# Kernel tuning notes

Hardware: AMD Instinct MI355X
Metric: run time of the kernel (lower is better)

## Reference

```python
import jax, jax.numpy as jnp
import numpy as np

NEG_BIG = -1e12
ALPHA = 0.2  # LeakyReLU negative slope

def setup_inputs() -> dict:
    key = jax.random.key(0)
    k1, k2, k3, k4, k5 = jax.random.split(key, 5)
    N, F_in, F_out = 8192, 256, 128
    inp = jax.random.normal(k1, (N, F_in), dtype=jnp.float32)
    adj = jax.random.randint(k2, (N, N), 0, 2, dtype=jnp.int32)
    W = jax.random.normal(k3, (F_in, F_out), dtype=jnp.float32) * 0.05
    W_2 = jax.random.normal(k4, (F_in, F_out), dtype=jnp.float32) * 0.05
    W_3 = jax.random.normal(k5, (F_in, F_out), dtype=jnp.float32) * 0.05
    return {"inp": inp, "adj": adj, "W": W, "W_2": W_2, "W_3": W_3}

def reference(inp, adj, W, W_2, W_3):
    # h = inp @ W, h_2 = inp @ W_2  -> scores e = LeakyReLU(h @ h_2^T)  [N, N]
    h = inp @ W
    h_2 = inp @ W_2
    e = jax.nn.leaky_relu(h @ h_2.T, negative_slope=ALPHA)
    # adjacency mask, row softmax (dropout disabled: eval mode)
    attention = jax.nn.softmax(jnp.where(adj > 0, e, NEG_BIG), axis=1)
    h_3 = inp @ W_3
    h_prime = attention @ h_3
    return jax.nn.elu(h_prime)  # concat=True path
```

## Files before the change

### kernel.cpp

```cpp
#include <hip/hip_runtime.h>
#include <hip/hip_fp16.h>

#define N    8192
#define FIN  256
#define FOUT 128
#define BN   64

typedef _Float16 half8 __attribute__((ext_vector_type(8)));
typedef _Float16 half4v __attribute__((ext_vector_type(4)));
typedef float floatx4 __attribute__((ext_vector_type(4)));

__global__ __launch_bounds__(256)
void wprep_kernel(const float* __restrict__ W0,
                  const float* __restrict__ W1,
                  const float* __restrict__ W2,
                  _Float16* __restrict__ Wf)
{
    int idx  = blockIdx.x * 256 + threadIdx.x;
    int lane = idx & 63;
    int frag = idx >> 6;
    int w    = frag >> 6;
    int f    = frag & 63;
    int nt   = f >> 3, kc = f & 7;
    int quad = lane >> 4, lo16 = lane & 15;
    const float* Wp = w == 0 ? W0 : (w == 1 ? W1 : W2);
    half8 v;
#pragma unroll
    for (int jj = 0; jj < 8; jj++)
        v[jj] = (_Float16)Wp[(size_t)(kc * 32 + quad * 8 + jj) * FOUT + nt * 16 + lo16];
    *(half8*)&Wf[(size_t)idx * 8] = v;
}

__global__ __launch_bounds__(256, 2)
void gemm3_kernel(const float* __restrict__ inp,
                  const _Float16* __restrict__ Wf,
                  _Float16* __restrict__ H,
                  _Float16* __restrict__ H2,
                  _Float16* __restrict__ H3T)
{
    const int which = blockIdx.z;
    const int c0    = blockIdx.y * 64;
    const _Float16* Wfw = Wf + (size_t)which * 64 * 64 * 8;
    const int r0 = blockIdx.x * 64;
    const int tid  = threadIdx.x;
    const int wave = tid >> 6;
    const int lane = tid & 63;
    const int lo16 = lane & 15;
    const int quad = lane >> 4;
    const int r = r0 + wave * 16 + lo16;

    half8 a[8];
#pragma unroll
    for (int kc = 0; kc < 8; kc++) {
        const float* p = &inp[(size_t)r * FIN + kc * 32 + quad * 8];
        float4 v0 = *(const float4*)p;
        float4 v1 = *(const float4*)(p + 4);
        a[kc][0] = (_Float16)v0.x; a[kc][1] = (_Float16)v0.y;
        a[kc][2] = (_Float16)v0.z; a[kc][3] = (_Float16)v0.w;
        a[kc][4] = (_Float16)v1.x; a[kc][5] = (_Float16)v1.y;
        a[kc][6] = (_Float16)v1.z; a[kc][7] = (_Float16)v1.w;
    }

    floatx4 acc[4];
#pragma unroll
    for (int i = 0; i < 4; i++) acc[i] = (floatx4){0.f, 0.f, 0.f, 0.f};

#pragma unroll
    for (int kc = 0; kc < 8; kc++)
#pragma unroll
        for (int nt = 0; nt < 4; nt++) {
            int ntg = (c0 >> 4) + nt;
            half8 b = *(const half8*)&Wfw[(((size_t)ntg * 8 + kc) * 64 + lane) * 8];
            acc[nt] = __builtin_amdgcn_mfma_f32_16x16x32_f16(a[kc], b, acc[nt], 0, 0, 0);
        }

    const int arow = wave * 16 + quad * 4;
    if (which < 2) {
        _Float16* outp = which == 0 ? H : H2;
#pragma unroll
        for (int nt = 0; nt < 4; nt++)
#pragma unroll
            for (int rr = 0; rr < 4; rr++)
                outp[(size_t)(r0 + arow + rr) * FOUT + c0 + nt * 16 + lo16] = (_Float16)acc[nt][rr];
    } else {
#pragma unroll
        for (int nt = 0; nt < 4; nt++) {
            half4v v;
#pragma unroll
            for (int rr = 0; rr < 4; rr++) v[rr] = (_Float16)acc[nt][rr];
            *(half4v*)&H3T[(size_t)(c0 + nt * 16 + lo16) * N + r0 + arow] = v;
        }
    }
}

__global__ __launch_bounds__(256)
void repackK_kernel(const _Float16* __restrict__ H2, _Float16* __restrict__ Kf)
{
    int idx  = blockIdx.x * 256 + threadIdx.x;
    int lane = idx & 63;
    int frag = idx >> 6;
    int jb = frag >> 4, f = frag & 15;
    int c = f >> 3, ntj = (f >> 2) & 1, kc = f & 3;
    int quad = lane >> 4, lo16 = lane & 15;
    int srcrow = jb * 64 + c * 32 + (lo16 >> 2) * 8 + ntj * 4 + (lo16 & 3);
    half8 v = *(const half8*)&H2[(size_t)srcrow * FOUT + kc * 32 + quad * 8];
    *(half8*)&Kf[(size_t)idx * 8] = v;
}

__global__ __launch_bounds__(256)
void repackV_kernel(const _Float16* __restrict__ H3T, _Float16* __restrict__ Vf)
{
    int idx  = blockIdx.x * 256 + threadIdx.x;
    int lane = idx & 63;
    int frag = idx >> 6;
    int jb = frag >> 4, f = frag & 15, nt = f >> 1, kc = f & 1;
    int quad = lane >> 4, lo16 = lane & 15;
    half8 v = *(const half8*)&H3T[(size_t)(nt * 16 + lo16) * N + jb * 64 + kc * 32 + quad * 8];
    *(half8*)&Vf[(size_t)idx * 8] = v;
}

template<int JS>
__global__ __launch_bounds__(256, 2)
void attn_kernel(const _Float16* __restrict__ Hq,
                 const _Float16* __restrict__ Kf,
                 const _Float16* __restrict__ Vf,
                 const int* __restrict__ adj,
                 float* __restrict__ OpartT,
                 float* __restrict__ mpart,
                 float* __restrict__ lpart)
{
    __shared__ _Float16 KV[2][16384];

    const int tid  = threadIdx.x;
    const int wave = tid >> 6;
    const int lane = tid & 63;
    const int lo16 = lane & 15;
    const int quad = lane >> 4;
    const int bid  = blockIdx.x;
    const int js   = bid & (JS - 1);
    const int ib   = bid / JS;
    const int i0   = ib * 128;
    const int iw   = i0 + wave * 32;
    const int jbeg = js * (N / JS);
    const int NIT  = (N / JS) / BN;

    half8 q[2][4];
#pragma unroll
    for (int isub = 0; isub < 2; isub++)
#pragma unroll
        for (int kc = 0; kc < 4; kc++)
            q[isub][kc] = *(const half8*)&Hq[(size_t)(iw + isub * 16 + lo16) * FOUT + kc * 32 + quad * 8];

    floatx4 O[8][2];
#pragma unroll
    for (int nt = 0; nt < 8; nt++)
#pragma unroll
        for (int s = 0; s < 2; s++) O[nt][s] = (floatx4){0.f, 0.f, 0.f, 0.f};
    float m_s[2] = {-1e12f, -1e12f}, l_s[2] = {0.f, 0.f};

    {
        const int jb0 = jbeg >> 6;
        const _Float16* gk = Kf + (size_t)jb0 * 8192;
        const _Float16* gv = Vf + (size_t)jb0 * 8192;
#pragma unroll
        for (int r = 0; r < 4; r++) {
            int off = (r * 256 + tid) * 8;
            *(half8*)&KV[0][off]        = *(const half8*)&gk[off];
            *(half8*)&KV[0][8192 + off] = *(const half8*)&gv[off];
        }
        __syncthreads();
    }

    int cur = 0;
    for (int it = 0; it < NIT; it++) {
        const int j0 = jbeg + it * BN;

        int av[32];
        {
            const int* ap = adj + (size_t)iw * N + j0 + lane;
#pragma unroll
            for (int x = 0; x < 32; x++) av[x] = ap[(size_t)x * N];
        }

        half8 st[8];
        if (it + 1 < NIT) {
            const int jbn = (j0 + BN) >> 6;
            const _Float16* gk = Kf + (size_t)jbn * 8192;
            const _Float16* gv = Vf + (size_t)jbn * 8192;
#pragma unroll
            for (int r = 0; r < 4; r++) {
                int off = (r * 256 + tid) * 8;
                st[r]     = *(const half8*)&gk[off];
                st[r + 4] = *(const half8*)&gv[off];
            }
        }

        const _Float16* kb = &KV[cur][0];
        const _Float16* vb = &KV[cur][8192];

        floatx4 S[2][2][2];
#pragma unroll
        for (int c = 0; c < 2; c++)
#pragma unroll
            for (int ntj = 0; ntj < 2; ntj++) {
                S[c][ntj][0] = (floatx4){0.f, 0.f, 0.f, 0.f};
                S[c][ntj][1] = (floatx4){0.f, 0.f, 0.f, 0.f};
#pragma unroll
                for (int kc = 0; kc < 4; kc++) {
                    half8 kf = *(const half8*)&kb[(((c * 2 + ntj) * 4 + kc) * 64 + lane) * 8];
                    S[c][ntj][0] = __builtin_amdgcn_mfma_f32_16x16x32_f16(kf, q[0][kc], S[c][ntj][0], 0, 0, 0);
                    S[c][ntj][1] = __builtin_amdgcn_mfma_f32_16x16x32_f16(kf, q[1][kc], S[c][ntj][1], 0, 0, 0);
                }
            }

        float alpha[2];
#pragma unroll
        for (int s = 0; s < 2; s++) {
            float mx = -1e12f;
#pragma unroll
            for (int c = 0; c < 2; c++)
#pragma unroll
                for (int ntj = 0; ntj < 2; ntj++)
#pragma unroll
                    for (int r = 0; r < 4; r++) {
                        float e = S[c][ntj][s][r];
                        e = e > 0.f ? e : 0.2f * e;
                        mx = fmaxf(mx, e);
                    }
            mx = fmaxf(mx, __shfl_xor(mx, 16));
            mx = fmaxf(mx, __shfl_xor(mx, 32));
            float mn = fmaxf(m_s[s], mx);
            alpha[s] = __expf(m_s[s] - mn);
            m_s[s] = mn;
        }

        unsigned long long mw0 = 0, mw1 = 0;
#pragma unroll
        for (int x = 0; x < 16; x++) {
            unsigned long long b0 = __ballot(av[x] != 0);
            unsigned long long b1 = __ballot(av[x + 16] != 0);
            bool sel = (lo16 == x);
            mw0 = sel ? b0 : mw0;
            mw1 = sel ? b1 : mw1;
        }
        unsigned long long mw[2] = {mw0, mw1};

        half8 pb[2][2];
        float sum[2] = {0.f, 0.f};
#pragma unroll
        for (int s = 0; s < 2; s++) {
            unsigned long long mq = mw[s] >> (quad * 8);
#pragma unroll
            for (int c = 0; c < 2; c++)
#pragma unroll
                for (int ntj = 0; ntj < 2; ntj++)
#pragma unroll
                    for (int r = 0; r < 4; r++) {
                        float e = S[c][ntj][s][r];
                        e = e > 0.f ? e : 0.2f * e;
                        bool bit = (mq >> (c * 32 + ntj * 4 + r)) & 1ull;
                        float p = bit ? __expf(e - m_s[s]) : 0.f;
                        sum[s] += p;
                        pb[s][c][ntj * 4 + r] = (_Float16)p;
                    }
            sum[s] += __shfl_xor(sum[s], 16);
            sum[s] += __shfl_xor(sum[s], 32);
            l_s[s] = l_s[s] * alpha[s] + sum[s];
#pragma unroll
            for (int nt = 0; nt < 8; nt++)
#pragma unroll
                for (int r = 0; r < 4; r++)
                    O[nt][s][r] *= alpha[s];
        }

#pragma unroll
        for (int c = 0; c < 2; c++)
#pragma unroll
            for (int nt = 0; nt < 8; nt++) {
                half8 vf = *(const half8*)&vb[((nt * 2 + c) * 64 + lane) * 8];
                O[nt][0] = __builtin_amdgcn_mfma_f32_16x16x32_f16(vf, pb[0][c], O[nt][0], 0, 0, 0);
                O[nt][1] = __builtin_amdgcn_mfma_f32_16x16x32_f16(vf, pb[1][c], O[nt][1], 0, 0, 0);
            }

        if (it + 1 < NIT) {
            const int nxt = cur ^ 1;
#pragma unroll
            for (int r = 0; r < 4; r++) {
                int off = (r * 256 + tid) * 8;
                *(half8*)&KV[nxt][off]        = st[r];
                *(half8*)&KV[nxt][8192 + off] = st[r + 4];
            }
        }
        __syncthreads();
        cur ^= 1;
    }

#pragma unroll
    for (int nt = 0; nt < 8; nt++)
#pragma unroll
        for (int s = 0; s < 2; s++)
#pragma unroll
            for (int r = 0; r < 4; r++) {
                int f = nt * 16 + quad * 4 + r;
                int i = iw + s * 16 + lo16;
                OpartT[((size_t)js * FOUT + f) * N + i] = O[nt][s][r];
            }
    if (quad == 0) {
#pragma unroll
        for (int s = 0; s < 2; s++) {
            mpart[js * N + iw + s * 16 + lo16] = m_s[s];
            lpart[js * N + iw + s * 16 + lo16] = l_s[s];
        }
    }
}

template<int JS>
__global__ __launch_bounds__(256)
void combine_kernel(const float* __restrict__ OpartT,
                    const float* __restrict__ mpart,
                    const float* __restrict__ lpart,
                    float* __restrict__ out)
{
    int idx = blockIdx.x * 256 + threadIdx.x;
    int f  = idx >> 11;
    int i4 = (idx & 2047) << 2;

    float4 M = {-3e38f, -3e38f, -3e38f, -3e38f};
    float4 m[JS];
#pragma unroll
    for (int s = 0; s < JS; s++) {
        m[s] = *(const float4*)&mpart[s * N + i4];
        M.x = fmaxf(M.x, m[s].x); M.y = fmaxf(M.y, m[s].y);
        M.z = fmaxf(M.z, m[s].z); M.w = fmaxf(M.w, m[s].w);
    }
    float4 L = {0.f, 0.f, 0.f, 0.f};
    float4 w[JS];
#pragma unroll
    for (int s = 0; s < JS; s++) {
        float4 l = *(const float4*)&lpart[s * N + i4];
        w[s].x = __expf(m[s].x - M.x); w[s].y = __expf(m[s].y - M.y);
        w[s].z = __expf(m[s].z - M.z); w[s].w = __expf(m[s].w - M.w);
        L.x += l.x * w[s].x; L.y += l.y * w[s].y;
        L.z += l.z * w[s].z; L.w += l.w * w[s].w;
    }
    float4 o = {0.f, 0.f, 0.f, 0.f};
#pragma unroll
    for (int s = 0; s < JS; s++) {
        float4 v = *(const float4*)&OpartT[((size_t)s * FOUT + f) * N + i4];
        o.x += w[s].x * v.x; o.y += w[s].y * v.y;
        o.z += w[s].z * v.z; o.w += w[s].w * v.w;
    }
    float r0 = o.x / L.x, r1 = o.y / L.y, r2 = o.z / L.z, r3 = o.w / L.w;
    out[(size_t)(i4 + 0) * FOUT + f] = r0 > 0.f ? r0 : __expf(r0) - 1.f;
    out[(size_t)(i4 + 1) * FOUT + f] = r1 > 0.f ? r1 : __expf(r1) - 1.f;
    out[(size_t)(i4 + 2) * FOUT + f] = r2 > 0.f ? r2 : __expf(r2) - 1.f;
    out[(size_t)(i4 + 3) * FOUT + f] = r3 > 0.f ? r3 : __expf(r3) - 1.f;
}

extern "C" void kernel_launch(void* const* d_in, const int* in_sizes, int n_in,
                              void* d_out, int out_size, void* d_ws, size_t ws_size,
                              hipStream_t stream) {
    const float* inp = (const float*)d_in[0];
    const int*   adj = (const int*)d_in[1];
    const float* W0  = (const float*)d_in[2];
    const float* W1  = (const float*)d_in[3];
    const float* W2  = (const float*)d_in[4];
    float* out = (float*)d_out;

    constexpr int JS = 8;
    char* ws = (char*)d_ws;
    _Float16* H    = (_Float16*)(ws);
    _Float16* H2   = (_Float16*)(ws + (2u << 20));
    _Float16* H3T  = (_Float16*)(ws + (4u << 20));
    _Float16* Wf   = (_Float16*)(ws + (6u << 20));
    _Float16* Kf   = (_Float16*)(ws + (7u << 20));
    _Float16* Vf   = (_Float16*)(ws + (9u << 20));
    float* OpartT  = (float*)(ws + (11u << 20));
    float* mpart   = (float*)(ws + (43u << 20));
    float* lpart   = (float*)(ws + (43u << 20) + (size_t)JS * N * sizeof(float));

    wprep_kernel<<<48, 256, 0, stream>>>(W0, W1, W2, Wf);
    gemm3_kernel<<<dim3(N / 64, 2, 3), 256, 0, stream>>>(inp, Wf, H, H2, H3T);
    repackK_kernel<<<512, 256, 0, stream>>>(H2, Kf);
    repackV_kernel<<<512, 256, 0, stream>>>(H3T, Vf);
    attn_kernel<JS><<<(N / 128) * JS, 256, 0, stream>>>(H, Kf, Vf, adj, OpartT, mpart, lpart);
    combine_kernel<JS><<<(FOUT * (N / 4)) / 256, 256, 0, stream>>>(OpartT, mpart, lpart, out);
}
```

Baseline: 432.6 us.

## Restructure attention kernel with direct-to-LDS K/V loads and vectorized adjacency reads

```diff
diff --git a/kernel.cpp b/kernel.cpp
--- a/kernel.cpp
+++ b/kernel.cpp
@@ -9,6 +9,10 @@
 typedef _Float16 half8 __attribute__((ext_vector_type(8)));
 typedef _Float16 half4v __attribute__((ext_vector_type(4)));
 typedef float floatx4 __attribute__((ext_vector_type(4)));
+
+#define GLDS(g, l) __builtin_amdgcn_global_load_lds(                        \
+    (const __attribute__((address_space(1))) void*)(g),                     \
+    (__attribute__((address_space(3))) void*)(l), 16, 0, 0)
 
 __global__ __launch_bounds__(256)
 void wprep_kernel(const float* __restrict__ W0,
@@ -120,7 +124,7 @@
 }
 
 template<int JS>
-__global__ __launch_bounds__(256, 2)
+__global__ __launch_bounds__(256, 3)
 void attn_kernel(const _Float16* __restrict__ Hq,
                  const _Float16* __restrict__ Kf,
                  const _Float16* __restrict__ Vf,
@@ -129,7 +133,7 @@
                  float* __restrict__ mpart,
                  float* __restrict__ lpart)
 {
-    __shared__ _Float16 KV[2][16384];
+    __shared__ _Float16 KV[16384];
 
     const int tid  = threadIdx.x;
     const int wave = tid >> 6;
@@ -139,83 +143,76 @@
     const int bid  = blockIdx.x;
     const int js   = bid & (JS - 1);
     const int ib   = bid / JS;
-    const int i0   = ib * 128;
-    const int iw   = i0 + wave * 32;
+    const int i0   = ib * 64;
+    const int iw   = i0 + wave * 16;
     const int jbeg = js * (N / JS);
-    const int NIT  = (N / JS) / BN;
-
-    half8 q[2][4];
-#pragma unroll
-    for (int isub = 0; isub < 2; isub++)
-#pragma unroll
-        for (int kc = 0; kc < 4; kc++)
-            q[isub][kc] = *(const half8*)&Hq[(size_t)(iw + isub * 16 + lo16) * FOUT + kc * 32 + quad * 8];
-
-    floatx4 O[8][2];
-#pragma unroll
-    for (int nt = 0; nt < 8; nt++)
-#pragma unroll
-        for (int s = 0; s < 2; s++) O[nt][s] = (floatx4){0.f, 0.f, 0.f, 0.f};
-    float m_s[2] = {-1e12f, -1e12f}, l_s[2] = {0.f, 0.f};
-
-    {
-        const int jb0 = jbeg >> 6;
-        const _Float16* gk = Kf + (size_t)jb0 * 8192;
-        const _Float16* gv = Vf + (size_t)jb0 * 8192;
-#pragma unroll
-        for (int r = 0; r < 4; r++) {
-            int off = (r * 256 + tid) * 8;
-            *(half8*)&KV[0][off]        = *(const half8*)&gk[off];
-            *(half8*)&KV[0][8192 + off] = *(const half8*)&gv[off];
-        }
-        __syncthreads();
-    }
-
-    int cur = 0;
-    for (int it = 0; it < NIT; it++) {
-        const int j0 = jbeg + it * BN;
-
-        int av[32];
-        {
-            const int* ap = adj + (size_t)iw * N + j0 + lane;
-#pragma unroll
-            for (int x = 0; x < 32; x++) av[x] = ap[(size_t)x * N];
-        }
-
-        half8 st[8];
-        if (it + 1 < NIT) {
-            const int jbn = (j0 + BN) >> 6;
-            const _Float16* gk = Kf + (size_t)jbn * 8192;
-            const _Float16* gv = Vf + (size_t)jbn * 8192;
+    const int NG   = (N / JS) / (BN * 4);
+
+    half8 q[4];
+#pragma unroll
+    for (int kc = 0; kc < 4; kc++)
+        q[kc] = *(const half8*)&Hq[(size_t)(iw + lo16) * FOUT + kc * 32 + quad * 8];
+
+    floatx4 O[8];
+#pragma unroll
+    for (int nt = 0; nt < 8; nt++) O[nt] = (floatx4){0.f, 0.f, 0.f, 0.f};
+    float m_r = -1e12f, l_r = 0.f;
+
+    const int* abase = adj + (size_t)iw * N + jbeg + 4 * lane;
+
+    for (int itg = 0; itg < NG; itg++) {
+        unsigned long long b64[4] = {0, 0, 0, 0};
+#pragma unroll
+        for (int half = 0; half < 2; half++) {
+            int4 av[8];
+#pragma unroll
+            for (int x = 0; x < 8; x++)
+                av[x] = *(const int4*)(abase + (size_t)(half * 8 + x) * N + itg * 256);
+#pragma unroll
+            for (int x = 0; x < 8; x++) {
+                unsigned long long bx = __ballot(av[x].x != 0);
+                unsigned long long by = __ballot(av[x].y != 0);
+                unsigned long long bz = __ballot(av[x].z != 0);
+                unsigned long long bw = __ballot(av[x].w != 0);
+                bool sel = (lo16 == half * 8 + x);
+                b64[0] = sel ? bx : b64[0];
+                b64[1] = sel ? by : b64[1];
+                b64[2] = sel ? bz : b64[2];
+                b64[3] = sel ? bw : b64[3];
+            }
+        }
+
+        #pragma unroll
+        for (int w = 0; w < 4; w++) {
+            const int jb = (jbeg + (itg * 4 + w) * BN) >> 6;
+            const _Float16* gk = Kf + (size_t)jb * 8192;
+            const _Float16* gv = Vf + (size_t)jb * 8192;
 #pragma unroll
             for (int r = 0; r < 4; r++) {
                 int off = (r * 256 + tid) * 8;
-                st[r]     = *(const half8*)&gk[off];
-                st[r + 4] = *(const half8*)&gv[off];
+                GLDS(gk + off, &KV[off]);
+                GLDS(gv + off, &KV[8192 + off]);
             }
-        }
-
-        const _Float16* kb = &KV[cur][0];
-        const _Float16* vb = &KV[cur][8192];
-
-        floatx4 S[2][2][2];
-#pragma unroll
-        for (int c = 0; c < 2; c++)
-#pragma unroll
-            for (int ntj = 0; ntj < 2; ntj++) {
-                S[c][ntj][0] = (floatx4){0.f, 0.f, 0.f, 0.f};
-                S[c][ntj][1] = (floatx4){0.f, 0.f, 0.f, 0.f};
-#pragma unroll
-                for (int kc = 0; kc < 4; kc++) {
-                    half8 kf = *(const half8*)&kb[(((c * 2 + ntj) * 4 + kc) * 64 + lane) * 8];
-                    S[c][ntj][0] = __builtin_amdgcn_mfma_f32_16x16x32_f16(kf, q[0][kc], S[c][ntj][0], 0, 0, 0);
-                    S[c][ntj][1] = __builtin_amdgcn_mfma_f32_16x16x32_f16(kf, q[1][kc], S[c][ntj][1], 0, 0, 0);
+            __syncthreads();
+
+            unsigned int mh[4];
+#pragma unroll
+            for (int r = 0; r < 4; r++)
+                mh[r] = (unsigned int)(b64[r] >> (w * 16)) & 0xffffu;
+
+            floatx4 S[2][2];
+#pragma unroll
+            for (int c = 0; c < 2; c++)
+#pragma unroll
+                for (int ntj = 0; ntj < 2; ntj++) {
+                    S[c][ntj] = (floatx4){0.f, 0.f, 0.f, 0.f};
+#pragma unroll
+                    for (int kc = 0; kc < 4; kc++) {
+                        half8 kf = *(const half8*)&KV[(((c * 2 + ntj) * 4 + kc) * 64 + lane) * 8];
+                        S[c][ntj] = __builtin_amdgcn_mfma_f32_16x16x32_f16(kf, q[kc], S[c][ntj], 0, 0, 0);
+                    }
                 }
-            }
-
-        float alpha[2];
-#pragma unroll
-        for (int s = 0; s < 2; s++) {
+
             float mx = -1e12f;
 #pragma unroll
             for (int c = 0; c < 2; c++)
@@ -223,94 +220,62 @@
                 for (int ntj = 0; ntj < 2; ntj++)
 #pragma unroll
                     for (int r = 0; r < 4; r++) {
-                        float e = S[c][ntj][s][r];
+                        float e = S[c][ntj][r];
                         e = e > 0.f ? e : 0.2f * e;
                         mx = fmaxf(mx, e);
                     }
             mx = fmaxf(mx, __shfl_xor(mx, 16));
             mx = fmaxf(mx, __shfl_xor(mx, 32));
-            float mn = fmaxf(m_s[s], mx);
-            alpha[s] = __expf(m_s[s] - mn);
-            m_s[s] = mn;
-        }
-
-        unsigned long long mw0 = 0, mw1 = 0;
-#pragma unroll
-        for (int x = 0; x < 16; x++) {
-            unsigned long long b0 = __ballot(av[x] != 0);
-            unsigned long long b1 = __ballot(av[x + 16] != 0);
-            bool sel = (lo16 == x);
-            mw0 = sel ? b0 : mw0;
-            mw1 = sel ? b1 : mw1;
-        }
-        unsigned long long mw[2] = {mw0, mw1};
-
-        half8 pb[2][2];
-        float sum[2] = {0.f, 0.f};
-#pragma unroll
-        for (int s = 0; s < 2; s++) {
-            unsigned long long mq = mw[s] >> (quad * 8);
+            float mn = fmaxf(m_r, mx);
+            float alpha = __expf(m_r - mn);
+            m_r = mn;
+
+            half8 pb[2];
+            float sum = 0.f;
 #pragma unroll
             for (int c = 0; c < 2; c++)
 #pragma unroll
                 for (int ntj = 0; ntj < 2; ntj++)
 #pragma unroll
                     for (int r = 0; r < 4; r++) {
-                        float e = S[c][ntj][s][r];
+                        float e = S[c][ntj][r];
                         e = e > 0.f ? e : 0.2f * e;
-                        bool bit = (mq >> (c * 32 + ntj * 4 + r)) & 1ull;
-                        float p = bit ? __expf(e - m_s[s]) : 0.f;
-                        sum[s] += p;
-                        pb[s][c][ntj * 4 + r] = (_Float16)p;
+                        bool bit = (mh[r] >> (c * 8 + quad * 2 + ntj)) & 1u;
+                        float p = bit ? __expf(e - m_r) : 0.f;
+                        sum += p;
+                        pb[c][ntj * 4 + r] = (_Float16)p;
                     }
-            sum[s] += __shfl_xor(sum[s], 16);
-            sum[s] += __shfl_xor(sum[s], 32);
-            l_s[s] = l_s[s] * alpha[s] + sum[s];
+            sum += __shfl_xor(sum, 16);
+            sum += __shfl_xor(sum, 32);
+            l_r = l_r * alpha + sum;
 #pragma unroll
             for (int nt = 0; nt < 8; nt++)
 #pragma unroll
                 for (int r = 0; r < 4; r++)
-                    O[nt][s][r] *= alpha[s];
-        }
-
-#pragma unroll
-        for (int c = 0; c < 2; c++)
-#pragma unroll
-            for (int nt = 0; nt < 8; nt++) {
-                half8 vf = *(const half8*)&vb[((nt * 2 + c) * 64 + lane) * 8];
-                O[nt][0] = __builtin_amdgcn_mfma_f32_16x16x32_f16(vf, pb[0][c], O[nt][0], 0, 0, 0);
-                O[nt][1] = __builtin_amdgcn_mfma_f32_16x16x32_f16(vf, pb[1][c], O[nt][1], 0, 0, 0);
-            }
-
-        if (it + 1 < NIT) {
-            const int nxt = cur ^ 1;
-#pragma unroll
-            for (int r = 0; r < 4; r++) {
-                int off = (r * 256 + tid) * 8;
-                *(half8*)&KV[nxt][off]        = st[r];
-                *(half8*)&KV[nxt][8192 + off] = st[r + 4];
-            }
-        }
-        __syncthreads();
-        cur ^= 1;
+                    O[nt][r] *= alpha;
+
+#pragma unroll
+            for (int c = 0; c < 2; c++)
+#pragma unroll
+                for (int nt = 0; nt < 8; nt++) {
+                    half8 vf = *(const half8*)&KV[8192 + ((nt * 2 + c) * 64 + lane) * 8];
+                    O[nt] = __builtin_amdgcn_mfma_f32_16x16x32_f16(vf, pb[c], O[nt], 0, 0, 0);
+                }
+
+            __syncthreads();
+        }
     }
 
 #pragma unroll
     for (int nt = 0; nt < 8; nt++)
 #pragma unroll
-        for (int s = 0; s < 2; s++)
-#pragma unroll
-            for (int r = 0; r < 4; r++) {
-                int f = nt * 16 + quad * 4 + r;
-                int i = iw + s * 16 + lo16;
-                OpartT[((size_t)js * FOUT + f) * N + i] = O[nt][s][r];
-            }
+        for (int r = 0; r < 4; r++) {
+            int f = nt * 16 + quad * 4 + r;
+            OpartT[((size_t)js * FOUT + f) * N + iw + lo16] = O[nt][r];
+        }
     if (quad == 0) {
-#pragma unroll
-        for (int s = 0; s < 2; s++) {
-            mpart[js * N + iw + s * 16 + lo16] = m_s[s];
-            lpart[js * N + iw + s * 16 + lo16] = l_s[s];
-        }
+        mpart[js * N + iw + lo16] = m_r;
+        lpart[js * N + iw + lo16] = l_r;
     }
 }
 
@@ -383,6 +348,6 @@
     gemm3_kernel<<<dim3(N / 64, 2, 3), 256, 0, stream>>>(inp, Wf, H, H2, H3T);
     repackK_kernel<<<512, 256, 0, stream>>>(H2, Kf);
     repackV_kernel<<<512, 256, 0, stream>>>(H3T, Vf);
-    attn_kernel<JS><<<(N / 128) * JS, 256, 0, stream>>>(H, Kf, Vf, adj, OpartT, mpart, lpart);
+    attn_kernel<JS><<<(N / 64) * JS, 256, 0, stream>>>(H, Kf, Vf, adj, OpartT, mpart, lpart);
     combine_kernel<JS><<<(FOUT * (N / 4)) / 256, 256, 0, stream>>>(OpartT, mpart, lpart, out);
 }
```

Measured after the change: 463.1 us. 7.1% more time.
